# Performance work log

Hardware: AMD Instinct MI355X
Metric: run time of the kernel (lower is better)

The kernel has to match this reference:

```python
import jax, jax.numpy as jnp
import numpy as np

B, S, H, A, F = 16, 512, 768, 12, 3072
DH = H // A  # 64
EPS = 1e-5

def layernorm(x, w, b):
    mu = jnp.mean(x, axis=-1, keepdims=True)
    var = jnp.mean(jnp.square(x - mu), axis=-1, keepdims=True)
    return (x - mu) * jax.lax.rsqrt(var + EPS) * w + b

def setup_inputs() -> dict:
    key = jax.random.key(0)
    ks = jax.random.split(key, 12)
    std = 0.02
    inp = {
        "X": jax.random.normal(ks[0], (B, S, H), jnp.float32),
        "mask": jax.random.randint(ks[1], (B, S), 0, 2, jnp.int32),
        "WQ": jax.random.normal(ks[2], (H, H), jnp.float32) * std,
        "bQ": jnp.zeros((H,), jnp.float32),
        "WK": jax.random.normal(ks[3], (H, H), jnp.float32) * std,
        "bK": jnp.zeros((H,), jnp.float32),
        "WV": jax.random.normal(ks[4], (H, H), jnp.float32) * std,
        "bV": jnp.zeros((H,), jnp.float32),
        "WO": jax.random.normal(ks[5], (H, H), jnp.float32) * std,
        "bO": jnp.zeros((H,), jnp.float32),
        "ln1_w": jnp.ones((H,), jnp.float32),
        "ln1_b": jnp.zeros((H,), jnp.float32),
        "W1": jax.random.normal(ks[6], (H, F), jnp.float32) * std,
        "b1": jnp.zeros((F,), jnp.float32),
        "W2": jax.random.normal(ks[7], (F, H), jnp.float32) * std,
        "b2": jnp.zeros((H,), jnp.float32),
        "ln2_w": jnp.ones((H,), jnp.float32),
        "ln2_b": jnp.zeros((H,), jnp.float32),
    }
    return inp

def reference(X, mask, WQ, bQ, WK, bK, WV, bV, WO, bO, ln1_w, ln1_b, W1, b1, W2, b2, ln2_w, ln2_b):
    # --- multi-head self-attention (pretrained-weights branch, faithful reshapes) ---
    Q = (X @ WQ + bQ).reshape(B, A, S, DH)
    K = (X @ WK + bK).reshape(B, A, S, DH)
    V = (X @ WV + bV).reshape(B, A, S, DH)
    scores = jnp.einsum('bhqd,bhkd->bhqk', Q, K) / jnp.sqrt(jnp.float32(DH))
    scores = jnp.where(mask[:, None, None, :] == 0, -jnp.inf, scores)
    attn = jax.nn.softmax(scores, axis=-1)
    Z = jnp.einsum('bhqk,bhkd->bhqd', attn, V).reshape(B, S, H)
    attn_out = Z @ WO + bO
    # residual + LN (dropout is identity in eval)
    X = layernorm(attn_out + X, ln1_w, ln1_b)
    # --- FFN with exact GELU ---
    ffn = jax.nn.gelu(X @ W1 + b1, approximate=False) @ W2 + b2
    X = layernorm(ffn + X, ln2_w, ln2_b)
    return X
```

## Files before the change

### kernel.cpp

```cpp
#include <hip/hip_runtime.h>
#include <hip/hip_bf16.h>


using bf16_t = __hip_bfloat16;
typedef __bf16 bf16x8 __attribute__((ext_vector_type(8)));
typedef float f32x4 __attribute__((ext_vector_type(4)));

__device__ __forceinline__ float b2f(bf16_t v) { return __bfloat162float(v); }
__device__ __forceinline__ bf16_t f2b(float v) { return __float2bfloat16(v); }
__device__ __forceinline__ ushort f2bu(float v) { bf16_t b = f2b(v); return *(ushort*)&b; }

__device__ __forceinline__ void glds16(const ushort* g, ushort* l) {
    __builtin_amdgcn_global_load_lds(
        (const __attribute__((address_space(1))) unsigned int*)g,
        (__attribute__((address_space(3))) unsigned int*)l, 16, 0, 0);
}

__device__ __forceinline__ float gelu_f(float x) {
    float x2 = x * x;
    float y2 = 1.5957691216057308f * x * fmaf(0.044715f, x2, 1.0f);
    float e = __expf(y2);
    float t = 1.f - 2.f / (e + 1.f);
    return 0.5f * x * (1.f + t);
}

__device__ __forceinline__ void tr_tile(const float* __restrict__ in,
                                        bf16_t* __restrict__ out,
                                        int R, int C, int tx, int ty,
                                        float (*t)[65], int tid)
{
    int r0 = ty * 64, c0 = tx * 64;
    int tr = tid >> 6, tc = tid & 63;
#pragma unroll 4
    for (int i = 0; i < 16; ++i) {
        int r = i * 4 + tr;
        t[r][tc] = in[(size_t)(r0 + r) * C + c0 + tc];
    }
    __syncthreads();
#pragma unroll 4
    for (int i = 0; i < 16; ++i) {
        int r = i * 4 + tr;
        out[(size_t)(c0 + r) * R + r0 + tc] = f2b(t[tc][r]);
    }
}

__global__ __launch_bounds__(256) void prep_kernel(
    const float* __restrict__ WQ, const float* __restrict__ WK,
    const float* __restrict__ WV, const float* __restrict__ WO,
    const float* __restrict__ W1, const float* __restrict__ W2,
    const float* __restrict__ bQ, const float* __restrict__ bK,
    const float* __restrict__ bV, const float* __restrict__ X,
    bf16_t* __restrict__ Wqkv, bf16_t* __restrict__ WOt,
    bf16_t* __restrict__ W1t, bf16_t* __restrict__ W2t,
    float* __restrict__ bcat, bf16_t* __restrict__ Xb)
{
    __shared__ float t[64][65];
    const int blk = blockIdx.x, tid = threadIdx.x;
    if (blk < 576) {
        int m = blk / 144, tt = blk % 144;
        const float* in = (m == 0) ? WQ : (m == 1) ? WK : (m == 2) ? WV : WO;
        bf16_t* out = (m == 0) ? Wqkv : (m == 1) ? Wqkv + 589824
                    : (m == 2) ? Wqkv + 1179648 : WOt;
        tr_tile(in, out, 768, 768, tt % 12, tt / 12, t, tid);
    } else if (blk < 1152) {
        int tt = blk - 576;
        tr_tile(W1, W1t, 768, 3072, tt % 48, tt / 48, t, tid);
    } else if (blk < 1728) {
        int tt = blk - 1152;
        tr_tile(W2, W2t, 3072, 768, tt % 12, tt / 12, t, tid);
    } else if (blk == 1728) {
        for (int i = tid; i < 2304; i += 256)
            bcat[i] = (i < 768) ? bQ[i] : (i < 1536) ? bK[i - 768] : bV[i - 1536];
    } else {
        size_t i = ((size_t)(blk - 1729) * 256 + tid) * 8;
        float4 a = *(const float4*)(X + i);
        float4 b = *(const float4*)(X + i + 4);
#pragma unroll
        for (int j = 0; j < 4; ++j) {
            Xb[i + j]     = f2b(((const float*)&a)[j]);
            Xb[i + 4 + j] = f2b(((const float*)&b)[j]);
        }
    }
}

__global__ __launch_bounds__(256) void transpose_bf(
    const ushort* __restrict__ in, ushort* __restrict__ out,
    int R, int C, long inB, long outB)
{
    __shared__ ushort t[64][65];
    const ushort* ip = in + (size_t)blockIdx.z * inB;
    ushort* op = out + (size_t)blockIdx.z * outB;
    int r0 = blockIdx.y * 64, c0 = blockIdx.x * 64;
    int tr = threadIdx.x >> 6, tc = threadIdx.x & 63;
#pragma unroll 4
    for (int i = 0; i < 16; ++i) {
        int r = i * 4 + tr;
        t[r][tc] = ip[(size_t)(r0 + r) * C + c0 + tc];
    }
    __syncthreads();
#pragma unroll 4
    for (int i = 0; i < 16; ++i) {
        int r = i * 4 + tr;
        op[(size_t)(c0 + r) * R + r0 + tc] = t[tc][r];
    }
}

template <int EPI, int NTILE>
__global__ __launch_bounds__(256) void gemm128(
    const bf16_t* __restrict__ A, const bf16_t* __restrict__ Bt,
    const float* __restrict__ bias, const void* __restrict__ res,
    void* __restrict__ Cv, int K, int lda, int ldb, int ldc)
{
    __shared__ ushort lA[128 * 64];
    __shared__ ushort lB[NTILE * 64];
    constexpr int NI = NTILE / 32;
    const int tid = threadIdx.x;
    const int l = tid & 63, w = tid >> 6;
    const int l16 = l & 15, quad = l >> 4;
    const int m0 = blockIdx.x * 128, n0 = blockIdx.y * NTILE;

    const int srow = tid >> 3;
    const int sg = (((tid & 7) ^ (srow & 7)) << 3);
    const ushort* gA = (const ushort*)A + (size_t)(m0 + srow) * lda + sg;
    const ushort* gB = (const ushort*)Bt + (size_t)(n0 + srow) * ldb + sg;
    ushort* dA = lA + tid * 8;
    ushort* dB = lB + tid * 8;

    f32x4 acc[4][NI] = {};
    const int arow = (w & 1) * 64;
    const int brow = (w >> 1) * (NTILE / 2);

    for (int k0 = 0; k0 < K; k0 += 64) {
        __syncthreads();
        glds16(gA + k0,                      dA);
        glds16(gA + k0 + (size_t)32 * lda,   dA + 2048);
        glds16(gA + k0 + (size_t)64 * lda,   dA + 4096);
        glds16(gA + k0 + (size_t)96 * lda,   dA + 6144);
        glds16(gB + k0,                      dB);
        glds16(gB + k0 + (size_t)32 * ldb,   dB + 2048);
        if constexpr (NTILE == 128) {
            glds16(gB + k0 + (size_t)64 * ldb, dB + 4096);
            glds16(gB + k0 + (size_t)96 * ldb, dB + 6144);
        }
        __syncthreads();
#pragma unroll
        for (int kk = 0; kk < 2; ++kk) {
            const int pc = (((kk * 4 + quad) ^ (l16 & 7)) << 3);
            bf16x8 bfr[NI];
#pragma unroll
            for (int ni = 0; ni < NI; ++ni)
                bfr[ni] = *(const bf16x8*)&lB[(brow + ni * 16 + l16) * 64 + pc];
#pragma unroll
            for (int mi = 0; mi < 4; ++mi) {
                bf16x8 afr = *(const bf16x8*)&lA[(arow + mi * 16 + l16) * 64 + pc];
#pragma unroll
                for (int ni = 0; ni < NI; ++ni)
                    acc[mi][ni] = __builtin_amdgcn_mfma_f32_16x16x32_bf16(afr, bfr[ni], acc[mi][ni], 0, 0, 0);
            }
        }
    }

    float bv[NI];
#pragma unroll
    for (int ni = 0; ni < NI; ++ni) bv[ni] = bias[n0 + brow + ni * 16 + l16];

    bf16_t* Cseg = nullptr;
    int nloc0 = 0;
    if constexpr (EPI == 6) {
        Cseg = (bf16_t*)Cv + (size_t)(n0 / 768) * 6291456;
        nloc0 = (n0 % 768) + brow;
    }

#pragma unroll
    for (int mi = 0; mi < 4; ++mi) {
#pragma unroll
        for (int ni = 0; ni < NI; ++ni) {
            int n = n0 + brow + ni * 16 + l16;
#pragma unroll
            for (int r = 0; r < 4; ++r) {
                int m = m0 + arow + mi * 16 + quad * 4 + r;
                float v = acc[mi][ni][r] + bv[ni];
                if constexpr (EPI == 1) {
                    v = gelu_f(v);
                } else if constexpr (EPI == 2) {
                    v += ((const float*)res)[(size_t)m * ldc + n];
                } else if constexpr (EPI == 5) {
                    v += b2f(((const bf16_t*)res)[(size_t)m * ldc + n]);
                }
                if constexpr (EPI == 5) {
                    ((float*)Cv)[(size_t)m * ldc + n] = v;
                } else if constexpr (EPI == 6) {
                    Cseg[(size_t)m * 768 + nloc0 + ni * 16 + l16] = f2b(v);
                } else {
                    ((bf16_t*)Cv)[(size_t)m * ldc + n] = f2b(v);
                }
            }
        }
    }
}

__global__ __launch_bounds__(256) void flash_kernel(
    const bf16_t* __restrict__ Q, const bf16_t* __restrict__ Kx,
    const bf16_t* __restrict__ Vt, const int* __restrict__ mask,
    bf16_t* __restrict__ Z)
{
    __shared__ ushort lK[64 * 64];
    __shared__ ushort lV[64 * 64];
    __shared__ ushort lP[64 * 72];

    const int h = blockIdx.y;
    const int q0 = blockIdx.x * 64;
    const ushort* Qh = (const ushort*)Q + (size_t)h * 32768;
    const ushort* Kh = (const ushort*)Kx + (size_t)h * 32768;
    const ushort* Vh = (const ushort*)Vt + (size_t)h * 32768;
    const int* mk = mask + (h / 12) * 512;
    ushort* Zh = (ushort*)Z + (size_t)h * 32768;

    const int tid = threadIdx.x;
    const int l = tid & 63, w = tid >> 6;
    const int l16 = l & 15, quad = l >> 4;

    bf16x8 qfr[2];
#pragma unroll
    for (int kk = 0; kk < 2; ++kk)
        qfr[kk] = *(const bf16x8*)(Qh + (size_t)(q0 + w * 16 + l16) * 64 + kk * 32 + quad * 8);

    const int c8p = tid & 7;
    const int kr0 = tid >> 3;
    float m_i[4] = {-1e30f, -1e30f, -1e30f, -1e30f};
    float l_i[4] = {0.f, 0.f, 0.f, 0.f};
    f32x4 o4[4] = {};

    for (int kt = 0; kt < 8; ++kt) {
#pragma unroll
        for (int p = 0; p < 2; ++p) {
            int row = kr0 + p * 32;
            int c8l = c8p ^ (row & 7);
            glds16(Kh + (size_t)(kt * 64 + row) * 64 + c8l * 8, lK + (p * 256 + tid) * 8);
            glds16(Vh + (size_t)row * 512 + kt * 64 + c8l * 8, lV + (p * 256 + tid) * 8);
        }
        __syncthreads();

        f32x4 s4[4] = {};
#pragma unroll
        for (int kk = 0; kk < 2; ++kk) {
#pragma unroll
            for (int nt = 0; nt < 4; ++nt) {
                int rr = nt * 16 + l16;
                bf16x8 bfr = *(const bf16x8*)&lK[rr * 64 + (((kk * 4 + quad) ^ (l16 & 7)) << 3)];
                s4[nt] = __builtin_amdgcn_mfma_f32_16x16x32_bf16(qfr[kk], bfr, s4[nt], 0, 0, 0);
            }
        }

        bool mz[4];
#pragma unroll
        for (int nt = 0; nt < 4; ++nt) mz[nt] = (mk[kt * 64 + nt * 16 + l16] == 0);
        float pv[4][4];
#pragma unroll
        for (int r = 0; r < 4; ++r) {
            float rm = -1e30f;
#pragma unroll
            for (int nt = 0; nt < 4; ++nt) {
                float v = mz[nt] ? -1e30f : s4[nt][r] * 0.125f;
                pv[nt][r] = v;
                rm = fmaxf(rm, v);
            }
#pragma unroll
            for (int off = 1; off < 16; off <<= 1) rm = fmaxf(rm, __shfl_xor(rm, off));
            float mn = fmaxf(m_i[r], rm);
            float al = __expf(m_i[r] - mn);
            float rs = 0.f;
#pragma unroll
            for (int nt = 0; nt < 4; ++nt) {
                float e = __expf(pv[nt][r] - mn);
                pv[nt][r] = e;
                rs += e;
            }
#pragma unroll
            for (int off = 1; off < 16; off <<= 1) rs += __shfl_xor(rs, off);
            l_i[r] = l_i[r] * al + rs;
            m_i[r] = mn;
#pragma unroll
            for (int dt = 0; dt < 4; ++dt) o4[dt][r] *= al;
        }

#pragma unroll
        for (int nt = 0; nt < 4; ++nt)
#pragma unroll
            for (int r = 0; r < 4; ++r)
                lP[(w * 16 + quad * 4 + r) * 72 + nt * 16 + l16] = f2bu(pv[nt][r]);
        __syncthreads();

#pragma unroll
        for (int kk = 0; kk < 2; ++kk) {
            bf16x8 pafr = *(const bf16x8*)&lP[(w * 16 + l16) * 72 + kk * 32 + quad * 8];
#pragma unroll
            for (int dt = 0; dt < 4; ++dt) {
                bf16x8 bvfr = *(const bf16x8*)&lV[(dt * 16 + l16) * 64 + (((kk * 4 + quad) ^ (l16 & 7)) << 3)];
                o4[dt] = __builtin_amdgcn_mfma_f32_16x16x32_bf16(pafr, bvfr, o4[dt], 0, 0, 0);
            }
        }
        __syncthreads();
    }

    float inv[4];
#pragma unroll
    for (int r = 0; r < 4; ++r) inv[r] = 1.f / l_i[r];
#pragma unroll
    for (int dt = 0; dt < 4; ++dt)
#pragma unroll
        for (int r = 0; r < 4; ++r)
            Zh[(size_t)(q0 + w * 16 + quad * 4 + r) * 64 + dt * 16 + l16] = f2bu(o4[dt][r] * inv[r]);
}

__device__ __forceinline__ float to_f(float v)  { return v; }
__device__ __forceinline__ float to_f(bf16_t v) { return b2f(v); }
__device__ __forceinline__ void from_f(float& d, float v)  { d = v; }
__device__ __forceinline__ void from_f(bf16_t& d, float v) { d = f2b(v); }

template <typename TI, typename TO>
__global__ __launch_bounds__(256) void layernorm_kernel(
    const TI* __restrict__ X, const float* __restrict__ w,
    const float* __restrict__ b, TO* __restrict__ out)
{
    const TI* x = X + (size_t)blockIdx.x * 768;
    TO* o = out + (size_t)blockIdx.x * 768;
    int t = threadIdx.x;
    float v[3];
    float s = 0.f, sq = 0.f;
#pragma unroll
    for (int i = 0; i < 3; ++i) {
        v[i] = to_f(x[t + i * 256]);
        s += v[i]; sq += v[i] * v[i];
    }
#pragma unroll
    for (int off = 32; off; off >>= 1) { s += __shfl_xor(s, off); sq += __shfl_xor(sq, off); }
    __shared__ float s1[4], s2[4];
    int wave = t >> 6, lane = t & 63;
    if (lane == 0) { s1[wave] = s; s2[wave] = sq; }
    __syncthreads();
    s  = s1[0] + s1[1] + s1[2] + s1[3];
    sq = s2[0] + s2[1] + s2[2] + s2[3];
    float mu  = s * (1.f / 768.f);
    float var = sq * (1.f / 768.f) - mu * mu;
    float rs  = rsqrtf(var + 1e-5f);
#pragma unroll
    for (int i = 0; i < 3; ++i)
        from_f(o[t + i * 256], (v[i] - mu) * rs * w[t + i * 256] + b[t + i * 256]);
}

extern "C" void kernel_launch(void* const* d_in, const int* in_sizes, int n_in,
                              void* d_out, int out_size, void* d_ws, size_t ws_size,
                              hipStream_t stream)
{
    const float* X    = (const float*)d_in[0];
    const int*   mask = (const int*)  d_in[1];
    const float* WQ   = (const float*)d_in[2];
    const float* bQ   = (const float*)d_in[3];
    const float* WK   = (const float*)d_in[4];
    const float* bK   = (const float*)d_in[5];
    const float* WV   = (const float*)d_in[6];
    const float* bV   = (const float*)d_in[7];
    const float* WO   = (const float*)d_in[8];
    const float* bO   = (const float*)d_in[9];
    const float* ln1w = (const float*)d_in[10];
    const float* ln1b = (const float*)d_in[11];
    const float* W1   = (const float*)d_in[12];
    const float* b1   = (const float*)d_in[13];
    const float* W2   = (const float*)d_in[14];
    const float* b2   = (const float*)d_in[15];
    const float* ln2w = (const float*)d_in[16];
    const float* ln2b = (const float*)d_in[17];
    float* out = (float*)d_out;

    bf16_t* ws   = (bf16_t*)d_ws;
    bf16_t* Wqkv = ws;
    bf16_t* WOt  = Wqkv + 1769472;
    bf16_t* W1t  = WOt + 589824;
    bf16_t* W2t  = W1t + 2359296;
    float*  bcat = (float*)(W2t + 2359296);
    bf16_t* Qb   = W2t + 2359296 + 4608;
    bf16_t* Kb   = Qb + 6291456;
    bf16_t* Vb   = Kb + 6291456;
    bf16_t* Xb   = Vb + 6291456;
    bf16_t* Vt   = Xb + 6291456;
    bf16_t* Zb = Qb;
    bf16_t* Y1 = Xb;
    bf16_t* X1 = Qb;
    bf16_t* Hb = Kb;

    prep_kernel<<<4801, 256, 0, stream>>>(WQ, WK, WV, WO, W1, W2, bQ, bK, bV, X,
                                          Wqkv, WOt, W1t, W2t, bcat, Xb);

    gemm128<6, 128><<<dim3(64, 18), 256, 0, stream>>>(Xb, Wqkv, bcat, nullptr, Qb,
                                                      768, 768, 768, 768);

    transpose_bf<<<dim3(1, 8, 192), 256, 0, stream>>>((const ushort*)Vb, (ushort*)Vt,
                                                      512, 64, 32768, 32768);

    flash_kernel<<<dim3(8, 192), 256, 0, stream>>>(Qb, Kb, Vt, mask, Zb);

    gemm128<2, 64><<<dim3(64, 12), 256, 0, stream>>>(Zb, WOt, bO, X, Y1,
                                                     768, 768, 768, 768);
    layernorm_kernel<bf16_t, bf16_t><<<8192, 256, 0, stream>>>(Y1, ln1w, ln1b, X1);

    gemm128<1, 128><<<dim3(64, 24), 256, 0, stream>>>(X1, W1t, b1, nullptr, Hb,
                                                      768, 768, 768, 3072);
    gemm128<5, 64><<<dim3(64, 12), 256, 0, stream>>>(Hb, W2t, b2, X1, out,
                                                     3072, 3072, 3072, 768);
    layernorm_kernel<float, float><<<8192, 256, 0, stream>>>(out, ln2w, ln2b, out);
}
```

Measured before the change: 370.0 us.

## Swap MFMA operands to transpose accumulators for vectorized epilogues and softmax

Swaps the A/B operands of the MFMA instructions in the GEMM and flash-attention kernels so each lane's four accumulator values lie along the N dimension instead of M. GEMM epilogues can then load bias and residual and store outputs as 4-wide vectors rather than scalar strided accesses. In attention, each lane now owns one query row, so the softmax needs two cross-quad shuffles instead of four-step reductions per row, and P and Z are written with ushort4 stores. The risk lies in the index arithmetic for the new accumulator layout and possible LDS bank conflicts on the P writes.

```diff
diff --git a/kernel.cpp b/kernel.cpp
--- a/kernel.cpp
+++ b/kernel.cpp
@@ -155,44 +155,48 @@
                 bf16x8 afr = *(const bf16x8*)&lA[(arow + mi * 16 + l16) * 64 + pc];
 #pragma unroll
                 for (int ni = 0; ni < NI; ++ni)
-                    acc[mi][ni] = __builtin_amdgcn_mfma_f32_16x16x32_bf16(afr, bfr[ni], acc[mi][ni], 0, 0, 0);
-            }
-        }
-    }
-
-    float bv[NI];
-#pragma unroll
-    for (int ni = 0; ni < NI; ++ni) bv[ni] = bias[n0 + brow + ni * 16 + l16];
-
-    bf16_t* Cseg = nullptr;
-    int nloc0 = 0;
-    if constexpr (EPI == 6) {
-        Cseg = (bf16_t*)Cv + (size_t)(n0 / 768) * 6291456;
-        nloc0 = (n0 % 768) + brow;
-    }
+                    acc[mi][ni] = __builtin_amdgcn_mfma_f32_16x16x32_bf16(bfr[ni], afr, acc[mi][ni], 0, 0, 0);
+            }
+        }
+    }
+
+    float4 bv4[NI];
+#pragma unroll
+    for (int ni = 0; ni < NI; ++ni)
+        bv4[ni] = *(const float4*)&bias[n0 + brow + ni * 16 + quad * 4];
 
 #pragma unroll
     for (int mi = 0; mi < 4; ++mi) {
+        int m = m0 + arow + mi * 16 + l16;
 #pragma unroll
         for (int ni = 0; ni < NI; ++ni) {
-            int n = n0 + brow + ni * 16 + l16;
-#pragma unroll
-            for (int r = 0; r < 4; ++r) {
-                int m = m0 + arow + mi * 16 + quad * 4 + r;
-                float v = acc[mi][ni][r] + bv[ni];
-                if constexpr (EPI == 1) {
-                    v = gelu_f(v);
-                } else if constexpr (EPI == 2) {
-                    v += ((const float*)res)[(size_t)m * ldc + n];
-                } else if constexpr (EPI == 5) {
-                    v += b2f(((const bf16_t*)res)[(size_t)m * ldc + n]);
-                }
-                if constexpr (EPI == 5) {
-                    ((float*)Cv)[(size_t)m * ldc + n] = v;
-                } else if constexpr (EPI == 6) {
-                    Cseg[(size_t)m * 768 + nloc0 + ni * 16 + l16] = f2b(v);
+            int nb = n0 + brow + ni * 16 + quad * 4;
+            float v[4];
+#pragma unroll
+            for (int r = 0; r < 4; ++r) v[r] = acc[mi][ni][r] + ((const float*)&bv4[ni])[r];
+            if constexpr (EPI == 1) {
+#pragma unroll
+                for (int r = 0; r < 4; ++r) v[r] = gelu_f(v[r]);
+            } else if constexpr (EPI == 2) {
+                float4 r4 = *(const float4*)&((const float*)res)[(size_t)m * ldc + nb];
+#pragma unroll
+                for (int r = 0; r < 4; ++r) v[r] += ((const float*)&r4)[r];
+            } else if constexpr (EPI == 5) {
+                ushort4 rb = *(const ushort4*)&((const ushort*)res)[(size_t)m * ldc + nb];
+#pragma unroll
+                for (int r = 0; r < 4; ++r) v[r] += b2f(*(const bf16_t*)&((const ushort*)&rb)[r]);
+            }
+            if constexpr (EPI == 5) {
+                *(float4*)&((float*)Cv)[(size_t)m * ldc + nb] = make_float4(v[0], v[1], v[2], v[3]);
+            } else {
+                ushort4 st;
+                st.x = f2bu(v[0]); st.y = f2bu(v[1]); st.z = f2bu(v[2]); st.w = f2bu(v[3]);
+                if constexpr (EPI == 6) {
+                    bf16_t* Cseg = (bf16_t*)Cv + (size_t)(n0 / 768) * 6291456;
+                    int nloc = (n0 % 768) + brow + ni * 16 + quad * 4;
+                    *(ushort4*)&((ushort*)Cseg)[(size_t)m * 768 + nloc] = st;
                 } else {
-                    ((bf16_t*)Cv)[(size_t)m * ldc + n] = f2b(v);
+                    *(ushort4*)&((ushort*)Cv)[(size_t)m * ldc + nb] = st;
                 }
             }
         }
@@ -227,8 +231,7 @@
 
     const int c8p = tid & 7;
     const int kr0 = tid >> 3;
-    float m_i[4] = {-1e30f, -1e30f, -1e30f, -1e30f};
-    float l_i[4] = {0.f, 0.f, 0.f, 0.f};
+    float m_i = -1e30f, l_i = 0.f;
     f32x4 o4[4] = {};
 
     for (int kt = 0; kt < 8; ++kt) {
@@ -246,49 +249,52 @@
         for (int kk = 0; kk < 2; ++kk) {
 #pragma unroll
             for (int nt = 0; nt < 4; ++nt) {
-                int rr = nt * 16 + l16;
-                bf16x8 bfr = *(const bf16x8*)&lK[rr * 64 + (((kk * 4 + quad) ^ (l16 & 7)) << 3)];
-                s4[nt] = __builtin_amdgcn_mfma_f32_16x16x32_bf16(qfr[kk], bfr, s4[nt], 0, 0, 0);
-            }
-        }
-
-        bool mz[4];
-#pragma unroll
-        for (int nt = 0; nt < 4; ++nt) mz[nt] = (mk[kt * 64 + nt * 16 + l16] == 0);
+                bf16x8 kfr = *(const bf16x8*)&lK[(nt * 16 + l16) * 64 + (((kk * 4 + quad) ^ (l16 & 7)) << 3)];
+                s4[nt] = __builtin_amdgcn_mfma_f32_16x16x32_bf16(kfr, qfr[kk], s4[nt], 0, 0, 0);
+            }
+        }
+
         float pv[4][4];
-#pragma unroll
-        for (int r = 0; r < 4; ++r) {
-            float rm = -1e30f;
-#pragma unroll
-            for (int nt = 0; nt < 4; ++nt) {
-                float v = mz[nt] ? -1e30f : s4[nt][r] * 0.125f;
+        float rm = -1e30f;
+#pragma unroll
+        for (int nt = 0; nt < 4; ++nt) {
+            int4 m4 = *(const int4*)&mk[kt * 64 + nt * 16 + quad * 4];
+#pragma unroll
+            for (int r = 0; r < 4; ++r) {
+                float v = (((const int*)&m4)[r] == 0) ? -1e30f : s4[nt][r] * 0.125f;
                 pv[nt][r] = v;
                 rm = fmaxf(rm, v);
             }
-#pragma unroll
-            for (int off = 1; off < 16; off <<= 1) rm = fmaxf(rm, __shfl_xor(rm, off));
-            float mn = fmaxf(m_i[r], rm);
-            float al = __expf(m_i[r] - mn);
-            float rs = 0.f;
-#pragma unroll
-            for (int nt = 0; nt < 4; ++nt) {
+        }
+        rm = fmaxf(rm, __shfl_xor(rm, 16));
+        rm = fmaxf(rm, __shfl_xor(rm, 32));
+        float mn = fmaxf(m_i, rm);
+        float al = __expf(m_i - mn);
+        float rs = 0.f;
+#pragma unroll
+        for (int nt = 0; nt < 4; ++nt)
+#pragma unroll
+            for (int r = 0; r < 4; ++r) {
                 float e = __expf(pv[nt][r] - mn);
                 pv[nt][r] = e;
                 rs += e;
             }
-#pragma unroll
-            for (int off = 1; off < 16; off <<= 1) rs += __shfl_xor(rs, off);
-            l_i[r] = l_i[r] * al + rs;
-            m_i[r] = mn;
-#pragma unroll
-            for (int dt = 0; dt < 4; ++dt) o4[dt][r] *= al;
-        }
-
-#pragma unroll
-        for (int nt = 0; nt < 4; ++nt)
-#pragma unroll
-            for (int r = 0; r < 4; ++r)
-                lP[(w * 16 + quad * 4 + r) * 72 + nt * 16 + l16] = f2bu(pv[nt][r]);
+        rs += __shfl_xor(rs, 16);
+        rs += __shfl_xor(rs, 32);
+        l_i = l_i * al + rs;
+        m_i = mn;
+#pragma unroll
+        for (int dt = 0; dt < 4; ++dt)
+#pragma unroll
+            for (int r = 0; r < 4; ++r) o4[dt][r] *= al;
+
+#pragma unroll
+        for (int nt = 0; nt < 4; ++nt) {
+            ushort4 st;
+            st.x = f2bu(pv[nt][0]); st.y = f2bu(pv[nt][1]);
+            st.z = f2bu(pv[nt][2]); st.w = f2bu(pv[nt][3]);
+            *(ushort4*)&lP[(w * 16 + l16) * 72 + nt * 16 + quad * 4] = st;
+        }
         __syncthreads();
 
 #pragma unroll
@@ -297,20 +303,20 @@
 #pragma unroll
             for (int dt = 0; dt < 4; ++dt) {
                 bf16x8 bvfr = *(const bf16x8*)&lV[(dt * 16 + l16) * 64 + (((kk * 4 + quad) ^ (l16 & 7)) << 3)];
-                o4[dt] = __builtin_amdgcn_mfma_f32_16x16x32_bf16(pafr, bvfr, o4[dt], 0, 0, 0);
+                o4[dt] = __builtin_amdgcn_mfma_f32_16x16x32_bf16(bvfr, pafr, o4[dt], 0, 0, 0);
             }
         }
         __syncthreads();
     }
 
-    float inv[4];
-#pragma unroll
-    for (int r = 0; r < 4; ++r) inv[r] = 1.f / l_i[r];
-#pragma unroll
-    for (int dt = 0; dt < 4; ++dt)
-#pragma unroll
-        for (int r = 0; r < 4; ++r)
-            Zh[(size_t)(q0 + w * 16 + quad * 4 + r) * 64 + dt * 16 + l16] = f2bu(o4[dt][r] * inv[r]);
+    float inv = 1.f / l_i;
+#pragma unroll
+    for (int dt = 0; dt < 4; ++dt) {
+        ushort4 st;
+        st.x = f2bu(o4[dt][0] * inv); st.y = f2bu(o4[dt][1] * inv);
+        st.z = f2bu(o4[dt][2] * inv); st.w = f2bu(o4[dt][3] * inv);
+        *(ushort4*)&Zh[(size_t)(q0 + w * 16 + l16) * 64 + dt * 16 + quad * 4] = st;
+    }
 }
 
 __device__ __forceinline__ float to_f(float v)  { return v; }
```

After: 379.7 us. +2.6%, slower.
